# Optimization experiments

Measured on AMD Instinct MI355X. Metric: run time of the kernel, lower is better.

## Reference

```python
import jax, jax.numpy as jnp
import numpy as np

N_NODES = 50000
N_EDGES = 500000
NEG_SLOPE = 0.2  # PyG GATConv default leaky_relu slope
EPS = 1e-16


def gat_conv(x, src, dst, W, a_src, a_dst, b, heads, ch):
    """PyG-style GATConv (concat=True), self-loops assumed already in src/dst."""
    n = x.shape[0]
    h = (x @ W).reshape(n, heads, ch)                      # [N,H,C]
    alpha_s = jnp.sum(h * a_src, axis=-1)                  # [N,H]
    alpha_d = jnp.sum(h * a_dst, axis=-1)                  # [N,H]
    e = jax.nn.leaky_relu(alpha_s[src] + alpha_d[dst], NEG_SLOPE)  # [E,H]
    m = jax.ops.segment_max(e, dst, num_segments=n)        # [N,H] segment softmax (stable)
    m = jnp.where(jnp.isfinite(m), m, 0.0)
    ex = jnp.exp(e - m[dst])
    den = jax.ops.segment_sum(ex, dst, num_segments=n)
    alpha = ex / (den[dst] + EPS)                          # [E,H]
    msg = h[src] * alpha[..., None]                        # [E,H,C] gather->weight
    out = jax.ops.segment_sum(msg, dst, num_segments=n)    # [N,H,C] scatter-add
    return out.reshape(n, heads * ch) + b


def setup_inputs() -> dict:
    key = jax.random.key(0)
    ks = jax.random.split(key, 11)
    s = 0.05
    return {
        "edge_index": jax.random.randint(ks[0], (2, N_EDGES), 0, N_NODES, dtype=jnp.int32),
        "batch_size": 8,
        "node_emb": jax.random.normal(ks[1], (N_NODES, 64), jnp.float32),
        "W1": jax.random.normal(ks[2], (64, 512), jnp.float32) * s,
        "att_src1": jax.random.normal(ks[3], (4, 128), jnp.float32) * s,
        "att_dst1": jax.random.normal(ks[4], (4, 128), jnp.float32) * s,
        "b1": jax.random.normal(ks[5], (512,), jnp.float32) * s,
        "W2": jax.random.normal(ks[6], (512, 256), jnp.float32) * s,
        "att_src2": jax.random.normal(ks[7], (1, 256), jnp.float32) * s,
        "att_dst2": jax.random.normal(ks[8], (1, 256), jnp.float32) * s,
        "b2": jax.random.normal(ks[9], (256,), jnp.float32) * s,
    }


def reference(edge_index, batch_size, node_emb, W1, att_src1, att_dst1, b1,
              W2, att_src2, att_dst2, b2):
    # add self-loops (PyG GATConv default add_self_loops=True)
    loops = jnp.arange(N_NODES, dtype=edge_index.dtype)
    src = jnp.concatenate([edge_index[0], loops])
    dst = jnp.concatenate([edge_index[1], loops])
    x = gat_conv(node_emb, src, dst, W1, att_src1, att_dst1, b1, heads=4, ch=128)
    x = jax.nn.elu(x)  # dropout inactive at eval
    x = gat_conv(x, src, dst, W2, att_src2, att_dst2, b2, heads=1, ch=256)
    g = jnp.mean(x, axis=0, keepdims=True)                 # [1, 256]
    return jnp.broadcast_to(g, (batch_size, g.shape[1]))
```

## Files before the change

kernel.cpp:

```cpp
#include <hip/hip_runtime.h>
#include <cstdint>

#define N_NODES 50000
#define N_EDGES 500000
#define ET (N_NODES + N_EDGES)
#define WSB 256
#define EBLK 2149
#define NEBLK 12500

typedef unsigned short u16;
typedef unsigned int   u32;
typedef __attribute__((ext_vector_type(8))) short short8;
typedef __attribute__((ext_vector_type(4))) float f32x4;

__device__ __forceinline__ float bf2f(u16 s) { return __uint_as_float((u32)s << 16); }
__device__ __forceinline__ u16 f2bf(float f) {
  u32 u = __float_as_uint(f);
  u32 r = (u + 0x7FFFu + ((u >> 16) & 1u)) >> 16;
  return (u16)r;
}
__device__ __forceinline__ void unpack8(uint4 u, float* f) {
  f[0] = __uint_as_float(u.x << 16); f[1] = __uint_as_float(u.x & 0xffff0000u);
  f[2] = __uint_as_float(u.y << 16); f[3] = __uint_as_float(u.y & 0xffff0000u);
  f[4] = __uint_as_float(u.z << 16); f[5] = __uint_as_float(u.z & 0xffff0000u);
  f[6] = __uint_as_float(u.w << 16); f[7] = __uint_as_float(u.w & 0xffff0000u);
}
__device__ __forceinline__ float lrelu(float v) { return v >= 0.f ? v : 0.2f * v; }

__device__ __forceinline__ int detect_fp32(const u16* __restrict__ ne) {
  int lane = threadIdx.x & 63;
  int bad = 0;
  #pragma unroll
  for (int j = 0; j < 2; ++j) {
    float v = fabsf(bf2f(ne[lane * 2 + j * 128]));
    bad += (!(v < 16.0f)) ? 1 : 0;
  }
  #pragma unroll
  for (int off = 32; off >= 1; off >>= 1) bad += __shfl_xor(bad, off, 64);
  return bad > 16;
}

__global__ __launch_bounds__(256) void k_prep(const int* __restrict__ ei,
                                              int* __restrict__ deg,
                                              const void* __restrict__ ne_src,
                                              u16* __restrict__ ne_b,
                                              const void* __restrict__ w1src,
                                              u16* __restrict__ W1t,
                                              const void* __restrict__ w2src,
                                              u16* __restrict__ W2t,
                                              const void* s0, const void* s1,
                                              const void* s2, const void* s3,
                                              const void* s4, const void* s5,
                                              float* d0, float* d1, float* d2,
                                              float* d3, float* d4, float* d5) {
  int b = blockIdx.x, tid = threadIdx.x;
  if (b < EBLK) {
    int e = b * 256 + tid;
    if (e < ET) {
      int d = (e < N_EDGES) ? ei[N_EDGES + e] : (e - N_EDGES);
      atomicAdd(&deg[d], 1);
    }
    return;
  }
  int fp32 = detect_fp32((const u16*)ne_src);
  b -= EBLK;
  if (b < NEBLK) {
    int i = b * 256 + tid;
    ne_b[i] = fp32 ? f2bf(((const float*)ne_src)[i]) : ((const u16*)ne_src)[i];
    return;
  }
  b -= NEBLK;
  if (b < 640) {
    int i = b * 256 + tid;
    if (i < 32768) {
      int n = i >> 6, k = i & 63;
      W1t[i] = fp32 ? f2bf(((const float*)w1src)[k * 512 + n])
                    : ((const u16*)w1src)[k * 512 + n];
    } else {
      int j = i - 32768;
      int n = j >> 9, k = j & 511;
      W2t[j] = fp32 ? f2bf(((const float*)w2src)[k * 256 + n])
                    : ((const u16*)w2src)[k * 256 + n];
    }
    return;
  }
  b -= 640;
  {
    int i = b * 256 + tid;
    const void* s; float* d; int j;
    if      (i < 512)  { s = s0; d = d0; j = i; }
    else if (i < 1024) { s = s1; d = d1; j = i - 512; }
    else if (i < 1536) { s = s2; d = d2; j = i - 1024; }
    else if (i < 1792) { s = s3; d = d3; j = i - 1536; }
    else if (i < 2048) { s = s4; d = d4; j = i - 1792; }
    else if (i < 2304) { s = s5; d = d5; j = i - 2048; }
    else return;
    d[j] = fp32 ? ((const float*)s)[j] : bf2f(((const u16*)s)[j]);
  }
}

__global__ void k_vab(const u16* __restrict__ W1t,
                      const float* __restrict__ as1v, const float* __restrict__ ad1v,
                      float* __restrict__ va_s, float* __restrict__ va_d,
                      const u16* __restrict__ W2t,
                      const float* __restrict__ as2v, const float* __restrict__ ad2v,
                      float* __restrict__ va2_s, float* __restrict__ va2_d) {
  if (blockIdx.x == 0) {
    int t = threadIdx.x;
    int h = t >> 6, k = t & 63;
    float s = 0.f, d = 0.f;
    for (int c = 0; c < 128; ++c) {
      float w = bf2f(W1t[(size_t)(h * 128 + c) * 64 + k]);
      s = fmaf(as1v[h * 128 + c], w, s);
      d = fmaf(ad1v[h * 128 + c], w, d);
    }
    va_s[t] = s;
    va_d[t] = d;
  } else {
    int k = (blockIdx.x - 1) * 256 + threadIdx.x;
    if (k >= 512) return;
    float s = 0.f, d = 0.f;
    for (int c = 0; c < 256; ++c) {
      float w = bf2f(W2t[(size_t)c * 512 + k]);
      s = fmaf(as2v[c], w, s);
      d = fmaf(ad2v[c], w, d);
    }
    va2_s[k] = s;
    va2_d[k] = d;
  }
}

__global__ __launch_bounds__(1024) void k_partial(const int* __restrict__ deg,
                                                  int* __restrict__ excl,
                                                  int* __restrict__ btot) {
  __shared__ int wsum[16];
  int tid = threadIdx.x;
  int i = blockIdx.x * 1024 + tid;
  int v = (i < N_NODES) ? deg[i] : 0;
  int lane = tid & 63, wid = tid >> 6;
  int incl = v;
  #pragma unroll
  for (int off = 1; off < 64; off <<= 1) {
    int t = __shfl_up(incl, off, 64);
    if (lane >= off) incl += t;
  }
  if (lane == 63) wsum[wid] = incl;
  __syncthreads();
  int prefix = 0;
  for (int w = 0; w < wid; ++w) prefix += wsum[w];
  if (i < N_NODES) excl[i] = prefix + incl - v;
  if (tid == 1023) btot[blockIdx.x] = prefix + incl;
}

__global__ void k_bases(const int* __restrict__ btot, int* __restrict__ bbase,
                        int* __restrict__ row_off, int nb) {
  int lane = threadIdx.x;
  int v = (lane < nb) ? btot[lane] : 0;
  int incl = v;
  #pragma unroll
  for (int off = 1; off < 64; off <<= 1) {
    int t = __shfl_up(incl, off, 64);
    if (lane >= off) incl += t;
  }
  if (lane < nb) bbase[lane] = incl - v;
  if (lane == 0) row_off[N_NODES] = ET;
}

__global__ __launch_bounds__(1024) void k_add(int* __restrict__ row_off,
                                              int* __restrict__ cursor,
                                              const int* __restrict__ bbase) {
  int i = blockIdx.x * 1024 + threadIdx.x;
  if (i < N_NODES) {
    int r = row_off[i] + bbase[blockIdx.x];
    row_off[i] = r;
    cursor[i] = r;
  }
}

__global__ __launch_bounds__(256) void k_scal(const int* __restrict__ ei,
                                              int* __restrict__ cursor,
                                              u16* __restrict__ srcs,
                                              const u16* __restrict__ ne_b,
                                              const float* __restrict__ va_s,
                                              const float* __restrict__ va_d,
                                              float* __restrict__ as_o,
                                              float* __restrict__ ad_o) {
  int b = blockIdx.x;
  if (b < EBLK) {
    int e = b * 256 + threadIdx.x;
    if (e >= ET) return;
    int s, d;
    if (e < N_EDGES) { s = ei[e]; d = ei[N_EDGES + e]; }
    else { s = d = e - N_EDGES; }
    int pos = atomicAdd(&cursor[d], 1);
    srcs[pos] = (u16)s;
    return;
  }
  b -= EBLK;
  int wid = threadIdx.x >> 6, lane = threadIdx.x & 63;
  int n = b * 4 + wid;
  if (n >= N_NODES) return;
  int h = lane >> 4, il = lane & 15;
  u32 u2[2];
  *(uint2*)u2 = *(const uint2*)(ne_b + (size_t)n * 64 + il * 4);
  float f[4];
  f[0] = bf2f((u16)u2[0]); f[1] = bf2f((u16)(u2[0] >> 16));
  f[2] = bf2f((u16)u2[1]); f[3] = bf2f((u16)(u2[1] >> 16));
  float4 vs = *(const float4*)(va_s + h * 64 + il * 4);
  float4 vd = *(const float4*)(va_d + h * 64 + il * 4);
  float s = f[0] * vs.x + f[1] * vs.y + f[2] * vs.z + f[3] * vs.w;
  float d = f[0] * vd.x + f[1] * vd.y + f[2] * vd.z + f[3] * vd.w;
  #pragma unroll
  for (int off = 8; off >= 1; off >>= 1) {
    s += __shfl_xor(s, off, 64);
    d += __shfl_xor(d, off, 64);
  }
  if (il == 0) { as_o[n * 4 + h] = s; ad_o[n * 4 + h] = d; }
}

#define LSTR 40
#define CPAD 136
__global__ __launch_bounds__(256) void k_gemm_l1(const u16* __restrict__ aggne,
                                                 const u16* __restrict__ W1t,
                                                 const float* __restrict__ b1f,
                                                 const float* __restrict__ va2_s,
                                                 const float* __restrict__ va2_d,
                                                 u16* __restrict__ x2,
                                                 float* __restrict__ as2,
                                                 float* __restrict__ ad2, int M) {
  __shared__ __align__(16) u16 smem[128 * CPAD];
  u16* As = smem;
  u16* Bs = smem + 128 * LSTR;
  const int tid = threadIdx.x;
  const int lane = tid & 63, wid = tid >> 6;
  const int wr = (wid >> 1) * 64, wc = (wid & 1) * 64;
  const int m = lane & 15, q = lane >> 4;
  const int row0 = blockIdx.x * 128, head = blockIdx.y;
  const u16* Bt = W1t + (size_t)head * 128 * 64;
  f32x4 acc[4][4] = {};
  #pragma unroll
  for (int kk = 0; kk < 64; kk += 32) {
    #pragma unroll
    for (int i = 0; i < 2; ++i) {
      int v = tid + i * 256;
      int row = v >> 2, ch = (v & 3) * 8;
      uint4 u = make_uint4(0, 0, 0, 0);
      int gr = row0 + row;
      if (gr < M) u = *(const uint4*)(aggne + (size_t)gr * 256 + head * 64 + kk + ch);
      *(uint4*)(As + row * LSTR + ch) = u;
    }
    #pragma unroll
    for (int i = 0; i < 2; ++i) {
      int v = tid + i * 256;
      int row = v >> 2, ch = (v & 3) * 8;
      uint4 u = *(const uint4*)(Bt + (size_t)row * 64 + kk + ch);
      *(uint4*)(Bs + row * LSTR + ch) = u;
    }
    __syncthreads();
    short8 af[4], bfr[4];
    #pragma unroll
    for (int t = 0; t < 4; ++t) {
      af[t]  = *(const short8*)(As + (wr + t * 16 + m) * LSTR + q * 8);
      bfr[t] = *(const short8*)(Bs + (wc + t * 16 + m) * LSTR + q * 8);
    }
    #pragma unroll
    for (int mt = 0; mt < 4; ++mt)
      #pragma unroll
      for (int nt = 0; nt < 4; ++nt)
        acc[mt][nt] = __builtin_amdgcn_mfma_f32_16x16x32_bf16(
            af[mt], bfr[nt], acc[mt][nt], 0, 0, 0);
    __syncthreads();
  }
  u16* Cs = smem;
  #pragma unroll
  for (int mt = 0; mt < 4; ++mt) {
    #pragma unroll
    for (int nt = 0; nt < 4; ++nt) {
      int lc = wc + nt * 16 + m;
      float bias = b1f[head * 128 + lc];
      #pragma unroll
      for (int r = 0; r < 4; ++r) {
        float v = acc[mt][nt][r] + bias;
        v = v > 0.f ? v : (__expf(v) - 1.0f);
        Cs[(wr + mt * 16 + q * 4 + r) * CPAD + lc] = f2bf(v);
      }
    }
  }
  __syncthreads();
  int row = tid >> 1, half = tid & 1;
  int gr = row0 + row;
  if (gr < M) {
    const u16* src = Cs + row * CPAD + half * 64;
    int cb = head * 128 + half * 64;
    float s = 0.f, d = 0.f;
    #pragma unroll
    for (int i = 0; i < 8; ++i) {
      uint4 u = *(const uint4*)(src + i * 8);
      *(uint4*)(x2 + (size_t)gr * 512 + cb + i * 8) = u;
      float f[8];
      unpack8(u, f);
      const float* pvs = va2_s + cb + i * 8;
      const float* pvd = va2_d + cb + i * 8;
      #pragma unroll
      for (int j = 0; j < 8; ++j) {
        s = fmaf(f[j], pvs[j], s);
        d = fmaf(f[j], pvd[j], d);
      }
    }
    s += __shfl_xor(s, 1, 64);
    d += __shfl_xor(d, 1, 64);
    if (half == 0) {
      atomicAdd(&as2[gr], s);
      atomicAdd(&ad2[gr], d);
    }
  }
}

__global__ __launch_bounds__(256) void k_fagg1(const int* __restrict__ row_off,
                                               const u16* __restrict__ srcs,
                                               const u16* __restrict__ ne_b,
                                               const float* __restrict__ as1,
                                               const float* __restrict__ ad1,
                                               u16* __restrict__ aggne) {
  int wid = threadIdx.x >> 6, lane = threadIdx.x & 63;
  int n = blockIdx.x * 4 + wid;
  if (n >= N_NODES) return;
  int start = row_off[n], end = row_off[n + 1];
  int g = lane >> 4, il = lane & 15;
  float adn_g = ad1[n * 4 + g];
  float sum = 0.f;
  for (int e0 = start; e0 < end; e0 += 16) {
    int e = e0 + il;
    if (e < end) sum += __expf(lrelu(as1[(int)srcs[e] * 4 + g] + adn_g));
  }
  #pragma unroll
  for (int off = 8; off >= 1; off >>= 1) sum += __shfl_xor(sum, off, 64);
  float inv = 1.0f / (sum + 1e-16f);
  float i_[4], d_[4];
  #pragma unroll
  for (int h = 0; h < 4; ++h) {
    i_[h] = __shfl(inv, h * 16, 64);
    d_[h] = __shfl(adn_g, h * 16, 64);
  }
  float acc[4] = {};
  for (int e0 = start; e0 < end; e0 += 64) {
    int lim = end - e0; if (lim > 64) lim = 64;
    int es = e0 + lane;
    int sreg = (int)srcs[es < end ? es : end - 1];
    float4 a = *(const float4*)(as1 + sreg * 4);
    float wreg[4];
    wreg[0] = __expf(lrelu(a.x + d_[0])) * i_[0];
    wreg[1] = __expf(lrelu(a.y + d_[1])) * i_[1];
    wreg[2] = __expf(lrelu(a.z + d_[2])) * i_[2];
    wreg[3] = __expf(lrelu(a.w + d_[3])) * i_[3];
    int j = 0;
    for (; j + 3 < lim; j += 4) {
      int sa = __shfl(sreg, j, 64),     sb = __shfl(sreg, j + 1, 64);
      int sc = __shfl(sreg, j + 2, 64), sd = __shfl(sreg, j + 3, 64);
      float f0 = bf2f(ne_b[(size_t)sa * 64 + lane]);
      float f1 = bf2f(ne_b[(size_t)sb * 64 + lane]);
      float f2 = bf2f(ne_b[(size_t)sc * 64 + lane]);
      float f3 = bf2f(ne_b[(size_t)sd * 64 + lane]);
      #pragma unroll
      for (int h = 0; h < 4; ++h) {
        acc[h] = fmaf(__shfl(wreg[h], j, 64), f0, acc[h]);
        acc[h] = fmaf(__shfl(wreg[h], j + 1, 64), f1, acc[h]);
        acc[h] = fmaf(__shfl(wreg[h], j + 2, 64), f2, acc[h]);
        acc[h] = fmaf(__shfl(wreg[h], j + 3, 64), f3, acc[h]);
      }
    }
    for (; j < lim; ++j) {
      int sa = __shfl(sreg, j, 64);
      float f0 = bf2f(ne_b[(size_t)sa * 64 + lane]);
      #pragma unroll
      for (int h = 0; h < 4; ++h)
        acc[h] = fmaf(__shfl(wreg[h], j, 64), f0, acc[h]);
    }
  }
  #pragma unroll
  for (int h = 0; h < 4; ++h)
    aggne[(size_t)n * 256 + h * 64 + lane] = f2bf(acc[h]);
}

__global__ __launch_bounds__(256) void k_nodew(const int* __restrict__ row_off,
                                               const u16* __restrict__ srcs,
                                               const float* __restrict__ as2,
                                               const float* __restrict__ ad2,
                                               float* __restrict__ c) {
  int wid = threadIdx.x >> 6, lane = threadIdx.x & 63;
  int n = blockIdx.x * 4 + wid;
  if (n >= N_NODES) return;
  int start = row_off[n], end = row_off[n + 1];
  int deg = end - start;
  float adn = ad2[n];
  if (deg <= 64) {
    int e = start + (lane < deg ? lane : 0);
    int s = (int)srcs[e];
    float ex = (lane < deg) ? __expf(lrelu(as2[s] + adn)) : 0.f;
    float sum = ex;
    #pragma unroll
    for (int off = 32; off >= 1; off >>= 1) sum += __shfl_xor(sum, off, 64);
    float w = ex / (sum + 1e-16f);
    if (lane < deg) atomicAdd(&c[s], w);
  } else {
    float sum = 0.f;
    for (int e = start + lane; e < end; e += 64)
      sum += __expf(lrelu(as2[(int)srcs[e]] + adn));
    #pragma unroll
    for (int off = 32; off >= 1; off >>= 1) sum += __shfl_xor(sum, off, 64);
    float inv = 1.0f / (sum + 1e-16f);
    for (int e = start + lane; e < end; e += 64) {
      int s = (int)srcs[e];
      float w = __expf(lrelu(as2[s] + adn)) * inv;
      atomicAdd(&c[s], w);
    }
  }
}

__global__ __launch_bounds__(256) void k_wsum(const u16* __restrict__ x2,
                                              const float* __restrict__ c,
                                              float* __restrict__ s_vec) {
  __shared__ float part[4][512];
  int wid = threadIdx.x >> 6, lane = threadIdx.x & 63;
  int wglob = blockIdx.x * 4 + wid;
  float acc[8] = {};
  int n = wglob;
  for (; n + WSB * 4 < N_NODES; n += WSB * 8) {
    int n2 = n + WSB * 4;
    float c0 = c[n], c1 = c[n2];
    uint4 u0 = *(const uint4*)(x2 + (size_t)n * 512 + lane * 8);
    uint4 u1 = *(const uint4*)(x2 + (size_t)n2 * 512 + lane * 8);
    float f0[8], f1[8];
    unpack8(u0, f0); unpack8(u1, f1);
    #pragma unroll
    for (int j = 0; j < 8; ++j) {
      acc[j] = fmaf(c0, f0[j], acc[j]);
      acc[j] = fmaf(c1, f1[j], acc[j]);
    }
  }
  if (n < N_NODES) {
    float c0 = c[n];
    uint4 u0 = *(const uint4*)(x2 + (size_t)n * 512 + lane * 8);
    float f0[8];
    unpack8(u0, f0);
    #pragma unroll
    for (int j = 0; j < 8; ++j) acc[j] = fmaf(c0, f0[j], acc[j]);
  }
  #pragma unroll
  for (int j = 0; j < 8; ++j) part[wid][lane * 8 + j] = acc[j];
  __syncthreads();
  int t = threadIdx.x;
  float v0 = part[0][t] + part[1][t] + part[2][t] + part[3][t];
  float v1 = part[0][t + 256] + part[1][t + 256] + part[2][t + 256] + part[3][t + 256];
  atomicAdd(&s_vec[t], v0);
  atomicAdd(&s_vec[t + 256], v1);
}

__global__ __launch_bounds__(256) void k_tinyfinal(const float* __restrict__ s_vec,
                                                   const u16* __restrict__ W2t,
                                                   const float* __restrict__ b2f,
                                                   float* __restrict__ out,
                                                   int out_size) {
  int wid = threadIdx.x >> 6, lane = threadIdx.x & 63;
  int cbase = blockIdx.x * 64 + wid * 16;
  float sv[8];
  #pragma unroll
  for (int j = 0; j < 8; ++j) sv[j] = s_vec[lane * 8 + j];
  for (int i = 0; i < 16; ++i) {
    int cc = cbase + i;
    uint4 u = *(const uint4*)(W2t + (size_t)cc * 512 + lane * 8);
    float f[8];
    unpack8(u, f);
    float p = 0.f;
    #pragma unroll
    for (int j = 0; j < 8; ++j) p = fmaf(sv[j], f[j], p);
    #pragma unroll
    for (int off = 32; off >= 1; off >>= 1) p += __shfl_xor(p, off, 64);
    if (lane == 0) {
      float val = p * (1.0f / (float)N_NODES) + b2f[cc];
      for (int o = cc; o < out_size; o += 256) out[o] = val;
    }
  }
}

extern "C" void kernel_launch(void* const* d_in, const int* in_sizes, int n_in,
                              void* d_out, int out_size, void* d_ws, size_t ws_size,
                              hipStream_t stream) {
  (void)in_sizes; (void)n_in; (void)ws_size;
  const int* edge_index = (const int*)d_in[0];
  float* out = (float*)d_out;

  char* w = (char*)d_ws;
  size_t off = 0;
  auto alloc = [&](size_t bytes) -> void* {
    void* p = w + off;
    off += (bytes + 255) & ~(size_t)255;
    return p;
  };
  u16*   ne_b    = (u16*)  alloc((size_t)N_NODES * 64 * 2);
  u16*   W1t     = (u16*)  alloc(32768 * 2);
  u16*   W2t     = (u16*)  alloc(131072 * 2);
  float* as1v    = (float*)alloc(512 * 4);
  float* ad1v    = (float*)alloc(512 * 4);
  float* b1f     = (float*)alloc(512 * 4);
  float* as2v    = (float*)alloc(256 * 4);
  float* ad2v    = (float*)alloc(256 * 4);
  float* b2f     = (float*)alloc(256 * 4);
  float* va_s    = (float*)alloc(256 * 4);
  float* va_d    = (float*)alloc(256 * 4);
  float* va2_s   = (float*)alloc(512 * 4);
  float* va2_d   = (float*)alloc(512 * 4);
  u16*   aggne   = (u16*)  alloc((size_t)N_NODES * 256 * 2);
  u16*   x2      = (u16*)  alloc((size_t)N_NODES * 512 * 2);
  float* as1     = (float*)alloc((size_t)N_NODES * 4 * 4);
  float* ad1     = (float*)alloc((size_t)N_NODES * 4 * 4);
  size_t z0 = off;
  float* as2     = (float*)alloc((size_t)N_NODES * 4);
  float* ad2     = (float*)alloc((size_t)N_NODES * 4);
  float* cwt     = (float*)alloc((size_t)N_NODES * 4);
  float* s_vec   = (float*)alloc(512 * 4);
  int*   deg     = (int*)  alloc((size_t)N_NODES * 4);
  size_t z1 = off;
  int*   row_off = (int*)  alloc((size_t)(N_NODES + 1) * 4);
  int*   cursor  = (int*)  alloc((size_t)N_NODES * 4);
  u16*   srcs    = (u16*)  alloc((size_t)ET * 2);
  int*   btot    = (int*)  alloc(64 * 4);
  int*   bbase   = (int*)  alloc(64 * 4);

  hipMemsetAsync(w + z0, 0, z1 - z0, stream);

  k_prep<<<EBLK + NEBLK + 640 + 9, 256, 0, stream>>>(
      edge_index, deg, d_in[2], ne_b, d_in[3], W1t, d_in[7], W2t,
      d_in[4], d_in[5], d_in[6], d_in[8], d_in[9], d_in[10],
      as1v, ad1v, b1f, as2v, ad2v, b2f);
  k_vab<<<3, 256, 0, stream>>>(W1t, as1v, ad1v, va_s, va_d,
                               W2t, as2v, ad2v, va2_s, va2_d);

  k_partial<<<49, 1024, 0, stream>>>(deg, row_off, btot);
  k_bases  <<<1, 64, 0, stream>>>(btot, bbase, row_off, 49);
  k_add    <<<49, 1024, 0, stream>>>(row_off, cursor, bbase);

  k_scal<<<EBLK + (N_NODES + 3) / 4, 256, 0, stream>>>(
      edge_index, cursor, srcs, ne_b, va_s, va_d, as1, ad1);

  k_fagg1<<<(N_NODES + 3) / 4, 256, 0, stream>>>(row_off, srcs, ne_b, as1, ad1, aggne);
  dim3 gl1((N_NODES + 127) / 128, 4);
  k_gemm_l1<<<gl1, 256, 0, stream>>>(aggne, W1t, b1f, va2_s, va2_d, x2, as2, ad2,
                                     N_NODES);

  k_nodew<<<(N_NODES + 3) / 4, 256, 0, stream>>>(row_off, srcs, as2, ad2, cwt);
  k_wsum<<<WSB, 256, 0, stream>>>(x2, cwt, s_vec);
  k_tinyfinal<<<4, 256, 0, stream>>>(s_vec, W2t, b2f, out, out_size);
}
```

Before: 306.2 us.

## Recompute layer-1 GEMM instead of materializing x2; fuse weighted node sum into GEMM

The layer-1 GEMM no longer writes the 50000x512 bf16 x2 tensor. One GEMM pass computes only the per-node attention scalars as2/ad2 from registers. A second identical GEMM pass, run after the node weights are known, folds the weighted column sum straight into s_vec, which removes the k_wsum kernel. This trades a duplicated small-K GEMM for avoiding a write and a re-read of about 50 MB. It also removes the shared-memory staging of the output tile.

```diff
diff --git a/kernel.cpp b/kernel.cpp
--- a/kernel.cpp
+++ b/kernel.cpp
@@ -4,7 +4,6 @@
 #define N_NODES 50000
 #define N_EDGES 500000
 #define ET (N_NODES + N_EDGES)
-#define WSB 256
 #define EBLK 2149
 #define NEBLK 12500
 
@@ -219,18 +218,15 @@
 }
 
 #define LSTR 40
-#define CPAD 136
-__global__ __launch_bounds__(256) void k_gemm_l1(const u16* __restrict__ aggne,
-                                                 const u16* __restrict__ W1t,
-                                                 const float* __restrict__ b1f,
-                                                 const float* __restrict__ va2_s,
-                                                 const float* __restrict__ va2_d,
-                                                 u16* __restrict__ x2,
-                                                 float* __restrict__ as2,
-                                                 float* __restrict__ ad2, int M) {
-  __shared__ __align__(16) u16 smem[128 * CPAD];
-  u16* As = smem;
-  u16* Bs = smem + 128 * LSTR;
+__global__ __launch_bounds__(256) void k_gemm_as2(const u16* __restrict__ aggne,
+                                                  const u16* __restrict__ W1t,
+                                                  const float* __restrict__ b1f,
+                                                  const float* __restrict__ va2_s,
+                                                  const float* __restrict__ va2_d,
+                                                  float* __restrict__ as2,
+                                                  float* __restrict__ ad2, int M) {
+  __shared__ __align__(16) u16 As[128 * LSTR];
+  __shared__ __align__(16) u16 Bs[128 * LSTR];
   const int tid = threadIdx.x;
   const int lane = tid & 63, wid = tid >> 6;
   const int wr = (wid >> 1) * 64, wc = (wid & 1) * 64;
@@ -271,49 +267,120 @@
             af[mt], bfr[nt], acc[mt][nt], 0, 0, 0);
     __syncthreads();
   }
-  u16* Cs = smem;
+  float vsr[4], vdr[4], br[4];
+  #pragma unroll
+  for (int nt = 0; nt < 4; ++nt) {
+    int cb = head * 128 + wc + nt * 16 + m;
+    br[nt] = b1f[cb]; vsr[nt] = va2_s[cb]; vdr[nt] = va2_d[cb];
+  }
   #pragma unroll
   for (int mt = 0; mt < 4; ++mt) {
-    #pragma unroll
-    for (int nt = 0; nt < 4; ++nt) {
-      int lc = wc + nt * 16 + m;
-      float bias = b1f[head * 128 + lc];
+    float sp[4] = {}, dp[4] = {};
+    #pragma unroll
+    for (int nt = 0; nt < 4; ++nt)
       #pragma unroll
       for (int r = 0; r < 4; ++r) {
-        float v = acc[mt][nt][r] + bias;
+        float v = acc[mt][nt][r] + br[nt];
         v = v > 0.f ? v : (__expf(v) - 1.0f);
-        Cs[(wr + mt * 16 + q * 4 + r) * CPAD + lc] = f2bf(v);
+        sp[r] = fmaf(v, vsr[nt], sp[r]);
+        dp[r] = fmaf(v, vdr[nt], dp[r]);
       }
-    }
-  }
+    #pragma unroll
+    for (int r = 0; r < 4; ++r) {
+      #pragma unroll
+      for (int off = 1; off <= 8; off <<= 1) {
+        sp[r] += __shfl_xor(sp[r], off, 64);
+        dp[r] += __shfl_xor(dp[r], off, 64);
+      }
+      int gr = row0 + wr + mt * 16 + q * 4 + r;
+      if (m == 0 && gr < M) {
+        atomicAdd(&as2[gr], sp[r]);
+        atomicAdd(&ad2[gr], dp[r]);
+      }
+    }
+  }
+}
+
+__global__ __launch_bounds__(256) void k_gemm_ws(const u16* __restrict__ aggne,
+                                                 const u16* __restrict__ W1t,
+                                                 const float* __restrict__ b1f,
+                                                 const float* __restrict__ cwt,
+                                                 float* __restrict__ s_vec, int M) {
+  __shared__ __align__(16) u16 As[128 * LSTR];
+  __shared__ __align__(16) u16 Bs[128 * LSTR];
+  __shared__ float part[128];
+  const int tid = threadIdx.x;
+  const int lane = tid & 63, wid = tid >> 6;
+  const int wr = (wid >> 1) * 64, wc = (wid & 1) * 64;
+  const int m = lane & 15, q = lane >> 4;
+  const int row0 = blockIdx.x * 128, head = blockIdx.y;
+  const u16* Bt = W1t + (size_t)head * 128 * 64;
+  f32x4 acc[4][4] = {};
+  #pragma unroll
+  for (int kk = 0; kk < 64; kk += 32) {
+    #pragma unroll
+    for (int i = 0; i < 2; ++i) {
+      int v = tid + i * 256;
+      int row = v >> 2, ch = (v & 3) * 8;
+      uint4 u = make_uint4(0, 0, 0, 0);
+      int gr = row0 + row;
+      if (gr < M) u = *(const uint4*)(aggne + (size_t)gr * 256 + head * 64 + kk + ch);
+      *(uint4*)(As + row * LSTR + ch) = u;
+    }
+    #pragma unroll
+    for (int i = 0; i < 2; ++i) {
+      int v = tid + i * 256;
+      int row = v >> 2, ch = (v & 3) * 8;
+      uint4 u = *(const uint4*)(Bt + (size_t)row * 64 + kk + ch);
+      *(uint4*)(Bs + row * LSTR + ch) = u;
+    }
+    __syncthreads();
+    short8 af[4], bfr[4];
+    #pragma unroll
+    for (int t = 0; t < 4; ++t) {
+      af[t]  = *(const short8*)(As + (wr + t * 16 + m) * LSTR + q * 8);
+      bfr[t] = *(const short8*)(Bs + (wc + t * 16 + m) * LSTR + q * 8);
+    }
+    #pragma unroll
+    for (int mt = 0; mt < 4; ++mt)
+      #pragma unroll
+      for (int nt = 0; nt < 4; ++nt)
+        acc[mt][nt] = __builtin_amdgcn_mfma_f32_16x16x32_bf16(
+            af[mt], bfr[nt], acc[mt][nt], 0, 0, 0);
+    __syncthreads();
+  }
+  if (tid < 128) part[tid] = 0.f;
+  float c_l = 0.f;
+  int crow = row0 + wr + lane;
+  if (crow < M) c_l = cwt[crow];
+  float cvr[16];
+  #pragma unroll
+  for (int mt = 0; mt < 4; ++mt)
+    #pragma unroll
+    for (int r = 0; r < 4; ++r)
+      cvr[mt * 4 + r] = __shfl(c_l, mt * 16 + q * 4 + r, 64);
   __syncthreads();
-  int row = tid >> 1, half = tid & 1;
-  int gr = row0 + row;
-  if (gr < M) {
-    const u16* src = Cs + row * CPAD + half * 64;
-    int cb = head * 128 + half * 64;
-    float s = 0.f, d = 0.f;
-    #pragma unroll
-    for (int i = 0; i < 8; ++i) {
-      uint4 u = *(const uint4*)(src + i * 8);
-      *(uint4*)(x2 + (size_t)gr * 512 + cb + i * 8) = u;
-      float f[8];
-      unpack8(u, f);
-      const float* pvs = va2_s + cb + i * 8;
-      const float* pvd = va2_d + cb + i * 8;
-      #pragma unroll
-      for (int j = 0; j < 8; ++j) {
-        s = fmaf(f[j], pvs[j], s);
-        d = fmaf(f[j], pvd[j], d);
+  float colacc[4] = {};
+  #pragma unroll
+  for (int nt = 0; nt < 4; ++nt) {
+    float b = b1f[head * 128 + wc + nt * 16 + m];
+    #pragma unroll
+    for (int mt = 0; mt < 4; ++mt)
+      #pragma unroll
+      for (int r = 0; r < 4; ++r) {
+        float v = acc[mt][nt][r] + b;
+        v = v > 0.f ? v : (__expf(v) - 1.0f);
+        colacc[nt] = fmaf(cvr[mt * 4 + r], v, colacc[nt]);
       }
-    }
-    s += __shfl_xor(s, 1, 64);
-    d += __shfl_xor(d, 1, 64);
-    if (half == 0) {
-      atomicAdd(&as2[gr], s);
-      atomicAdd(&ad2[gr], d);
-    }
-  }
+  }
+  #pragma unroll
+  for (int nt = 0; nt < 4; ++nt) {
+    colacc[nt] += __shfl_xor(colacc[nt], 16, 64);
+    colacc[nt] += __shfl_xor(colacc[nt], 32, 64);
+    if (q == 0) atomicAdd(&part[wc + nt * 16 + m], colacc[nt]);
+  }
+  __syncthreads();
+  if (tid < 128) atomicAdd(&s_vec[head * 128 + tid], part[tid]);
 }
 
 __global__ __launch_bounds__(256) void k_fagg1(const int* __restrict__ row_off,
@@ -415,45 +482,6 @@
       atomicAdd(&c[s], w);
     }
   }
-}
-
-__global__ __launch_bounds__(256) void k_wsum(const u16* __restrict__ x2,
-                                              const float* __restrict__ c,
-                                              float* __restrict__ s_vec) {
-  __shared__ float part[4][512];
-  int wid = threadIdx.x >> 6, lane = threadIdx.x & 63;
-  int wglob = blockIdx.x * 4 + wid;
-  float acc[8] = {};
-  int n = wglob;
-  for (; n + WSB * 4 < N_NODES; n += WSB * 8) {
-    int n2 = n + WSB * 4;
-    float c0 = c[n], c1 = c[n2];
-    uint4 u0 = *(const uint4*)(x2 + (size_t)n * 512 + lane * 8);
-    uint4 u1 = *(const uint4*)(x2 + (size_t)n2 * 512 + lane * 8);
-    float f0[8], f1[8];
-    unpack8(u0, f0); unpack8(u1, f1);
-    #pragma unroll
-    for (int j = 0; j < 8; ++j) {
-      acc[j] = fmaf(c0, f0[j], acc[j]);
-      acc[j] = fmaf(c1, f1[j], acc[j]);
-    }
-  }
-  if (n < N_NODES) {
-    float c0 = c[n];
-    uint4 u0 = *(const uint4*)(x2 + (size_t)n * 512 + lane * 8);
-    float f0[8];
-    unpack8(u0, f0);
-    #pragma unroll
-    for (int j = 0; j < 8; ++j) acc[j] = fmaf(c0, f0[j], acc[j]);
-  }
-  #pragma unroll
-  for (int j = 0; j < 8; ++j) part[wid][lane * 8 + j] = acc[j];
-  __syncthreads();
-  int t = threadIdx.x;
-  float v0 = part[0][t] + part[1][t] + part[2][t] + part[3][t];
-  float v1 = part[0][t + 256] + part[1][t + 256] + part[2][t + 256] + part[3][t + 256];
-  atomicAdd(&s_vec[t], v0);
-  atomicAdd(&s_vec[t + 256], v1);
 }
 
 __global__ __launch_bounds__(256) void k_tinyfinal(const float* __restrict__ s_vec,
@@ -511,7 +539,6 @@
   float* va2_s   = (float*)alloc(512 * 4);
   float* va2_d   = (float*)alloc(512 * 4);
   u16*   aggne   = (u16*)  alloc((size_t)N_NODES * 256 * 2);
-  u16*   x2      = (u16*)  alloc((size_t)N_NODES * 512 * 2);
   float* as1     = (float*)alloc((size_t)N_NODES * 4 * 4);
   float* ad1     = (float*)alloc((size_t)N_NODES * 4 * 4);
   size_t z0 = off;
@@ -545,10 +572,10 @@
 
   k_fagg1<<<(N_NODES + 3) / 4, 256, 0, stream>>>(row_off, srcs, ne_b, as1, ad1, aggne);
   dim3 gl1((N_NODES + 127) / 128, 4);
-  k_gemm_l1<<<gl1, 256, 0, stream>>>(aggne, W1t, b1f, va2_s, va2_d, x2, as2, ad2,
-                                     N_NODES);
+  k_gemm_as2<<<gl1, 256, 0, stream>>>(aggne, W1t, b1f, va2_s, va2_d, as2, ad2,
+                                      N_NODES);
 
   k_nodew<<<(N_NODES + 3) / 4, 256, 0, stream>>>(row_off, srcs, as2, ad2, cwt);
-  k_wsum<<<WSB, 256, 0, stream>>>(x2, cwt, s_vec);
+  k_gemm_ws<<<gl1, 256, 0, stream>>>(aggne, W1t, b1f, cwt, s_vec, N_NODES);
   k_tinyfinal<<<4, 256, 0, stream>>>(s_vec, W2t, b2f, out, out_size);
 }
```

Result: faster. 297.7 us (-2.8%).
